# Optimization experiments

Hardware: AMD Instinct MI355X
Metric: run time of the kernel (lower is better)

## Reference

```python
import jax, jax.numpy as jnp
import numpy as np

B, L, D = 4, 4096, 256
INIT_ALPHA = -2.0
INV_TEMP = 1.0 / 0.1


def setup_inputs() -> dict:
    key = jax.random.key(0)
    k1, k2, k3, k4 = jax.random.split(key, 4)
    latents = jax.random.normal(k1, (B, L, D), dtype=jnp.float32)
    current_coords = jax.random.normal(k2, (B, L, 2), dtype=jnp.float32)
    # Linear(D, D, bias=False) weights (torch stores [out, in]; y = x @ W.T)
    lim = 1.0 / np.sqrt(D)
    Wq = jax.random.uniform(k3, (D, D), minval=-lim, maxval=lim, dtype=jnp.float32)
    Wk = jax.random.uniform(k4, (D, D), minval=-lim, maxval=lim, dtype=jnp.float32)
    alpha_raw = jnp.asarray(INIT_ALPHA, dtype=jnp.float32)
    return {"latents": latents, "current_coords": current_coords,
            "Wq": Wq, "Wk": Wk, "alpha_raw": alpha_raw, "layer_idx": 3}


def _l2norm(x, eps=1e-12):
    # F.normalize(dim=-1): x / max(||x||, eps)
    n = jnp.sqrt(jnp.sum(x * x, axis=-1, keepdims=True))
    return x / jnp.maximum(n, eps)


def reference(latents, current_coords, Wq, Wk, alpha_raw, layer_idx):
    # pred_idx selection (share_weights=True): 0 if layer_idx==0 else 1;
    # layer_idx=3 -> params given are for pred_idx=1.
    q = _l2norm(jnp.einsum('bld,ed->ble', latents, Wq))  # [B,L,D]
    k = _l2norm(jnp.einsum('bld,ed->ble', latents, Wk))  # [B,L,D]
    scores = jnp.einsum('bld,bmd->blm', q, k) * INV_TEMP  # [B,L,L]
    scores = jnp.clip(scores, -50.0, 50.0)
    W = jax.nn.softmax(scores, axis=-1)                   # [B,L,L]
    alpha = jax.nn.sigmoid(alpha_raw)
    # M = alpha*W + (1-alpha)*I; M @ coords == alpha*(W@coords) + (1-alpha)*coords
    new_coords = alpha * jnp.einsum('blm,bmc->blc', W, current_coords) \
                 + (1.0 - alpha) * current_coords
    displacement = new_coords - current_coords
    return (new_coords, displacement)
```

## Files before the change

### kernel.cpp

```cpp
#include <hip/hip_runtime.h>
#include <hip/hip_bf16.h>

#define BB 4
#define LL 4096
#define DD 256
#define MM (BB * LL)
#define NSPLIT 8
#define BM 256
#define NQB (LL / BM)
#define KPS (LL / NSPLIT)
#define KT 64
#define NKT (KPS / KT)

typedef short short8 __attribute__((ext_vector_type(8)));
typedef float floatx4 __attribute__((ext_vector_type(4)));

#define SCALE_LOG2E 14.426950408889634f


__device__ __forceinline__ unsigned short f2bf(float f) {
    __hip_bfloat16 h = __float2bfloat16(f);
    union { __hip_bfloat16 h; unsigned short s; } c; c.h = h; return c.s;
}

__device__ __forceinline__ float fast_exp2(float x) {
#if __has_builtin(__builtin_amdgcn_exp2f)
    return __builtin_amdgcn_exp2f(x);
#else
    return exp2f(x);
#endif
}

__device__ __forceinline__ void stage16(const char* g, char* l, int lane) {
#if __has_builtin(__builtin_amdgcn_global_load_lds)
    __builtin_amdgcn_global_load_lds(
        (const __attribute__((address_space(1))) void*)(g + lane * 16),
        (__attribute__((address_space(3))) void*)l, 16, 0, 0);
#else
    *(short8*)(l + lane * 16) = *(const short8*)(g + lane * 16);
#endif
}

__global__ __launch_bounds__(256) void cvt_fm_kernel(
    const float* __restrict__ srcq, const float* __restrict__ srck,
    unsigned short* __restrict__ dstq, unsigned short* __restrict__ dstk)
{
    const int which = blockIdx.x >> 5;
    const float* src = which ? srck : srcq;
    unsigned short* dst = which ? dstk : dstq;
    const int t = (blockIdx.x & 31) * 256 + threadIdx.x;
    const int r = t >> 5, c = t & 31;
    const float4 v0 = ((const float4*)src)[t * 2];
    const float4 v1 = ((const float4*)src)[t * 2 + 1];
    short8 o;
    o[0] = (short)f2bf(v0.x); o[1] = (short)f2bf(v0.y);
    o[2] = (short)f2bf(v0.z); o[3] = (short)f2bf(v0.w);
    o[4] = (short)f2bf(v1.x); o[5] = (short)f2bf(v1.y);
    o[6] = (short)f2bf(v1.z); o[7] = (short)f2bf(v1.w);
    const int chunk = (r >> 4) * 512 + c * 16 + (r & 15);
    *(short8*)(dst + (size_t)chunk * 8) = o;
}

__global__ __launch_bounds__(256) void proj_norm_kernel(
    const float* __restrict__ latents,
    const __hip_bfloat16* __restrict__ Wq,
    const __hip_bfloat16* __restrict__ Wk,
    __hip_bfloat16* __restrict__ qn,
    __hip_bfloat16* __restrict__ kn)
{
    __shared__ char lds[65536];

    const int tid  = threadIdx.x;
    const int wave = tid >> 6;
    const int lane = tid & 63;
    const int n15  = lane & 15;
    const int quad = lane >> 4;

    const int pass  = (blockIdx.x >> 3) & 1;
    const int pidx  = (blockIdx.x & 7) | ((blockIdx.x >> 4) << 3);
    const int rbase = pidx * 64;
    const int m0    = rbase + wave * 16;
    const int r160  = rbase >> 4;

    short8 afrag[8];
    const float* Abase = latents + (size_t)(m0 + n15) * DD + quad * 8;
#pragma unroll
    for (int kk = 0; kk < 8; ++kk) {
        const float4 v0 = *(const float4*)(Abase + kk * 32);
        const float4 v1 = *(const float4*)(Abase + kk * 32 + 4);
        short8 f;
        f[0] = (short)f2bf(v0.x); f[1] = (short)f2bf(v0.y);
        f[2] = (short)f2bf(v0.z); f[3] = (short)f2bf(v0.w);
        f[4] = (short)f2bf(v1.x); f[5] = (short)f2bf(v1.y);
        f[6] = (short)f2bf(v1.z); f[7] = (short)f2bf(v1.w);
        afrag[kk] = f;
    }

    const char* W = (const char*)(pass ? Wk : Wq);

    floatx4 acc[16];
#pragma unroll
    for (int ct = 0; ct < 16; ++ct) acc[ct] = (floatx4){0.f, 0.f, 0.f, 0.f};

    {
        const char* src = W + wave * 8192;
        char* dst = lds + wave * 8192;
#pragma unroll
        for (int j = 0; j < 8; ++j) stage16(src + j * 1024, dst + j * 1024, lane);
    }

    for (int round = 0; round < 4; ++round) {
        __syncthreads();
        if (round + 1 < 4) {
            const char* src = W + (size_t)(round + 1) * 32768 + wave * 8192;
            char* dst = lds + ((round + 1) & 1) * 32768 + wave * 8192;
#pragma unroll
            for (int j = 0; j < 8; ++j) stage16(src + j * 1024, dst + j * 1024, lane);
        }
        const char* buf = lds + (round & 1) * 32768;
#pragma unroll
        for (int jt = 0; jt < 4; ++jt) {
            const int ct = round * 4 + jt;
            const char* lbase = buf + jt * 8192 + lane * 16;
            floatx4 a = acc[ct];
            __builtin_amdgcn_s_setprio(1);
#pragma unroll
            for (int kk = 0; kk < 8; ++kk) {
                short8 bfr = *(const short8*)(lbase + kk * 1024);
                a = __builtin_amdgcn_mfma_f32_16x16x32_bf16(afrag[kk], bfr, a, 0, 0, 0);
            }
            __builtin_amdgcn_s_setprio(0);
            acc[ct] = a;
        }
    }

    float ss[4] = {0.f, 0.f, 0.f, 0.f};
#pragma unroll
    for (int ct = 0; ct < 16; ++ct)
#pragma unroll
        for (int r = 0; r < 4; ++r) ss[r] += acc[ct][r] * acc[ct][r];
#pragma unroll
    for (int r = 0; r < 4; ++r) {
        ss[r] += __shfl_xor(ss[r], 1, 64);
        ss[r] += __shfl_xor(ss[r], 2, 64);
        ss[r] += __shfl_xor(ss[r], 4, 64);
        ss[r] += __shfl_xor(ss[r], 8, 64);
    }
    float sc[4];
#pragma unroll
    for (int r = 0; r < 4; ++r) {
        sc[r] = 1.f / fmaxf(sqrtf(ss[r]), 1e-12f);
        if (pass == 0) sc[r] *= SCALE_LOG2E;
    }

    __hip_bfloat16* dstp = pass ? kn : qn;
    unsigned short* tb = (unsigned short*)lds;
#pragma unroll
    for (int h = 0; h < 2; ++h) {
        __syncthreads();
#pragma unroll
        for (int cth = 0; cth < 8; ++cth) {
            const int ct = h * 8 + cth;
            const int col = cth * 16 + n15;
#pragma unroll
            for (int r = 0; r < 4; ++r) {
                const int rl = wave * 16 + quad * 4 + r;
                tb[rl * 136 + col] = f2bf(acc[ct][r] * sc[r]);
            }
        }
        __syncthreads();
#pragma unroll
        for (int j = 0; j < 4; ++j) {
            const int g = tid + j * 256;
            const int n15r = g & 15, q2 = (g >> 4) & 3, kkh = (g >> 6) & 3, r16l = (g >> 8) & 3;
            const int rl = r16l * 16 + n15r;
            short8 v = *(const short8*)(tb + rl * 136 + kkh * 32 + q2 * 8);
            const size_t chunk = (((size_t)(r160 + r16l) * 8 + (h * 4 + kkh)) * 4 + q2) * 16 + n15r;
            *(short8*)((char*)dstp + chunk * 16) = v;
        }
    }
}

__global__ __launch_bounds__(512) void attn_kernel(
    const __hip_bfloat16* __restrict__ qn,
    const __hip_bfloat16* __restrict__ kn,
    const float* __restrict__ coords,
    float* __restrict__ partials)
{
    __shared__ char lds[2 * 32768];

    const int tid  = threadIdx.x;
    const int wave = tid >> 6;
    const int lane = tid & 63;
    const int n15  = lane & 15;
    const int quad = lane >> 4;

    int bs = (blockIdx.x & 7) * 64 + (blockIdx.x >> 3);
    const int qb    = bs % NQB;    bs /= NQB;
    const int split = bs % NSPLIT; bs /= NSPLIT;
    const int b     = bs;

    const int mw = b * LL + qb * BM + wave * 32;

    const int key_base = b * LL + split * KPS;
    const char* ksrc = (const char*)kn + (size_t)key_base * 512;

    {
        const char* src = ksrc + wave * 4096;
        char* dst = lds + wave * 4096;
#pragma unroll
        for (int j = 0; j < 4; ++j) stage16(src + j * 1024, dst + j * 1024, lane);
    }

    short8 aq[2][8];
    const int t16 = mw >> 4;
#pragma unroll
    for (int rt = 0; rt < 2; ++rt)
#pragma unroll
        for (int kk = 0; kk < 8; ++kk) {
            const size_t chunk = (((size_t)(t16 + rt) * 8 + kk) * 4 + quad) * 16 + n15;
            aq[rt][kk] = *(const short8*)((const char*)qn + chunk * 16);
        }

    float s0[2][4], s1[2][4], s2[2][4];
#pragma unroll
    for (int rt = 0; rt < 2; ++rt)
#pragma unroll
        for (int r = 0; r < 4; ++r) { s0[rt][r] = 0.f; s1[rt][r] = 0.f; s2[rt][r] = 0.f; }

    for (int kt = 0; kt < NKT; ++kt) {
        __syncthreads();
        if (kt + 1 < NKT) {
            const char* src = ksrc + (size_t)(kt + 1) * KT * 512 + wave * 4096;
            char* dst = lds + ((kt + 1) & 1) * 32768 + wave * 4096;
#pragma unroll
            for (int j = 0; j < 4; ++j) stage16(src + j * 1024, dst + j * 1024, lane);
        }
        const char* buf = lds + (kt & 1) * 32768;

#pragma unroll
        for (int ct = 0; ct < 4; ++ct) {
            const int kidx = key_base + kt * KT + ct * 16 + n15;
            const float2 cc = *(const float2*)(coords + (size_t)kidx * 2);

            floatx4 acc[2][2];
#pragma unroll
            for (int rt = 0; rt < 2; ++rt)
#pragma unroll
                for (int hh = 0; hh < 2; ++hh) acc[rt][hh] = (floatx4){0.f, 0.f, 0.f, 0.f};
            const char* lbase = buf + ct * 8192 + lane * 16;
#pragma unroll
            for (int kk = 0; kk < 8; ++kk) {
                const short8 bfr = *(const short8*)(lbase + kk * 1024);
                acc[0][kk >> 2] = __builtin_amdgcn_mfma_f32_16x16x32_bf16(aq[0][kk], bfr, acc[0][kk >> 2], 0, 0, 0);
                acc[1][kk >> 2] = __builtin_amdgcn_mfma_f32_16x16x32_bf16(aq[1][kk], bfr, acc[1][kk >> 2], 0, 0, 0);
            }
#pragma unroll
            for (int r = 0; r < 4; ++r) {
                const float e0 = fast_exp2(acc[0][0][r] + acc[0][1][r]);
                const float e1 = fast_exp2(acc[1][0][r] + acc[1][1][r]);
                s0[0][r] += e0;
                s1[0][r] = fmaf(cc.x, e0, s1[0][r]);
                s2[0][r] = fmaf(cc.y, e0, s2[0][r]);
                s0[1][r] += e1;
                s1[1][r] = fmaf(cc.x, e1, s1[1][r]);
                s2[1][r] = fmaf(cc.y, e1, s2[1][r]);
            }
        }
    }

#pragma unroll
    for (int rt = 0; rt < 2; ++rt)
#pragma unroll
        for (int r = 0; r < 4; ++r)
#pragma unroll
            for (int mask = 1; mask <= 8; mask <<= 1) {
                s0[rt][r] += __shfl_xor(s0[rt][r], mask, 64);
                s1[rt][r] += __shfl_xor(s1[rt][r], mask, 64);
                s2[rt][r] += __shfl_xor(s2[rt][r], mask, 64);
            }

    if (n15 == 0) {
#pragma unroll
        for (int rt = 0; rt < 2; ++rt)
#pragma unroll
            for (int r = 0; r < 4; ++r) {
                const int m = mw + rt * 16 + quad * 4 + r;
                float* p = partials + ((size_t)split * MM + m) * 4;
                p[0] = s0[rt][r];
                p[1] = s1[rt][r];
                p[2] = s2[rt][r];
            }
    }
}

__global__ __launch_bounds__(256) void finish_kernel(
    const float* __restrict__ partials,
    const float* __restrict__ coords,
    const float* __restrict__ alpha_raw,
    float* __restrict__ out)
{
    const int m = blockIdx.x * 256 + threadIdx.x;

    const float alpha = 1.f / (1.f + __expf(-alpha_raw[0]));

    float s0 = 0.f, s1 = 0.f, s2 = 0.f;
#pragma unroll
    for (int s = 0; s < NSPLIT; ++s) {
        const float4 v = *(const float4*)(partials + ((size_t)s * MM + m) * 4);
        s0 += v.x; s1 += v.y; s2 += v.z;
    }

    const float cx = coords[m * 2];
    const float cy = coords[m * 2 + 1];
    const float inv = 1.f / s0;
    const float nx = alpha * (s1 * inv) + (1.f - alpha) * cx;
    const float ny = alpha * (s2 * inv) + (1.f - alpha) * cy;

    out[m * 2]     = nx;
    out[m * 2 + 1] = ny;
    out[2 * MM + m * 2]     = nx - cx;
    out[2 * MM + m * 2 + 1] = ny - cy;
}

extern "C" void kernel_launch(void* const* d_in, const int* in_sizes, int n_in,
                              void* d_out, int out_size, void* d_ws, size_t ws_size,
                              hipStream_t stream) {
    const float* latents   = (const float*)d_in[0];
    const float* coords    = (const float*)d_in[1];
    const float* Wq        = (const float*)d_in[2];
    const float* Wk        = (const float*)d_in[3];
    const float* alpha_raw = (const float*)d_in[4];

    char* ws = (char*)d_ws;
    __hip_bfloat16* qn   = (__hip_bfloat16*)ws;
    __hip_bfloat16* kn   = (__hip_bfloat16*)(ws + (size_t)8 * 1024 * 1024);
    __hip_bfloat16* wq_b = (__hip_bfloat16*)(ws + (size_t)16 * 1024 * 1024);
    __hip_bfloat16* wk_b = (__hip_bfloat16*)(ws + (size_t)16 * 1024 * 1024 + 131072);
    float* partials      = (float*)(ws + (size_t)16 * 1024 * 1024 + 262144);

    float* out = (float*)d_out;

    cvt_fm_kernel<<<64, 256, 0, stream>>>(Wq, Wk, (unsigned short*)wq_b, (unsigned short*)wk_b);
    proj_norm_kernel<<<512, 256, 0, stream>>>(latents, wq_b, wk_b, qn, kn);
    attn_kernel<<<BB * NQB * NSPLIT, 512, 0, stream>>>(qn, kn, coords, partials);
    finish_kernel<<<MM / 256, 256, 0, stream>>>(partials, coords, alpha_raw, out);
}
```

Before: 129.9 us.

## Stage coords in LDS, batch MFMAs over two key tiles with setprio

Each block's coordinate slice for its key split is copied into LDS once at kernel start, so the inner loop no longer issues a global float2 load per 16-key tile. The MFMA chain now runs over two key tiles before the exp/accumulate phase. Each tile uses a single accumulator per row tile instead of two split halves that were added afterwards. s_setprio brackets the MFMA section so waves in that section get issue priority, aiming to overlap matrix work with other waves' exp math. The cost is a longer single dependent MFMA chain per accumulator and slightly more LDS.

```diff
diff --git a/kernel.cpp b/kernel.cpp
--- a/kernel.cpp
+++ b/kernel.cpp
@@ -187,7 +187,8 @@
     const float* __restrict__ coords,
     float* __restrict__ partials)
 {
-    __shared__ char lds[2 * 32768];
+    __shared__ char lds[2 * 32768 + 4096];
+    char* clds = lds + 2 * 32768;
 
     const int tid  = threadIdx.x;
     const int wave = tid >> 6;
@@ -205,6 +206,10 @@
     const int key_base = b * LL + split * KPS;
     const char* ksrc = (const char*)kn + (size_t)key_base * 512;
 
+    if (wave < 4)
+        stage16((const char*)coords + (size_t)key_base * 8 + wave * 1024,
+                clds + wave * 1024, lane);
+
     {
         const char* src = ksrc + wave * 4096;
         char* dst = lds + wave * 4096;
@@ -239,32 +244,41 @@
         const char* buf = lds + (kt & 1) * 32768;
 
 #pragma unroll
-        for (int ct = 0; ct < 4; ++ct) {
-            const int kidx = key_base + kt * KT + ct * 16 + n15;
-            const float2 cc = *(const float2*)(coords + (size_t)kidx * 2);
-
+        for (int ch = 0; ch < 2; ++ch) {
             floatx4 acc[2][2];
 #pragma unroll
-            for (int rt = 0; rt < 2; ++rt)
-#pragma unroll
-                for (int hh = 0; hh < 2; ++hh) acc[rt][hh] = (floatx4){0.f, 0.f, 0.f, 0.f};
-            const char* lbase = buf + ct * 8192 + lane * 16;
-#pragma unroll
-            for (int kk = 0; kk < 8; ++kk) {
-                const short8 bfr = *(const short8*)(lbase + kk * 1024);
-                acc[0][kk >> 2] = __builtin_amdgcn_mfma_f32_16x16x32_bf16(aq[0][kk], bfr, acc[0][kk >> 2], 0, 0, 0);
-                acc[1][kk >> 2] = __builtin_amdgcn_mfma_f32_16x16x32_bf16(aq[1][kk], bfr, acc[1][kk >> 2], 0, 0, 0);
-            }
-#pragma unroll
-            for (int r = 0; r < 4; ++r) {
-                const float e0 = fast_exp2(acc[0][0][r] + acc[0][1][r]);
-                const float e1 = fast_exp2(acc[1][0][r] + acc[1][1][r]);
-                s0[0][r] += e0;
-                s1[0][r] = fmaf(cc.x, e0, s1[0][r]);
-                s2[0][r] = fmaf(cc.y, e0, s2[0][r]);
-                s0[1][r] += e1;
-                s1[1][r] = fmaf(cc.x, e1, s1[1][r]);
-                s2[1][r] = fmaf(cc.y, e1, s2[1][r]);
+            for (int ctl = 0; ctl < 2; ++ctl)
+#pragma unroll
+                for (int rt = 0; rt < 2; ++rt) acc[ctl][rt] = (floatx4){0.f, 0.f, 0.f, 0.f};
+
+            __builtin_amdgcn_s_setprio(1);
+#pragma unroll
+            for (int ctl = 0; ctl < 2; ++ctl) {
+                const char* lbase = buf + (ch * 2 + ctl) * 8192 + lane * 16;
+#pragma unroll
+                for (int kk = 0; kk < 8; ++kk) {
+                    const short8 bfr = *(const short8*)(lbase + kk * 1024);
+                    acc[ctl][0] = __builtin_amdgcn_mfma_f32_16x16x32_bf16(aq[0][kk], bfr, acc[ctl][0], 0, 0, 0);
+                    acc[ctl][1] = __builtin_amdgcn_mfma_f32_16x16x32_bf16(aq[1][kk], bfr, acc[ctl][1], 0, 0, 0);
+                }
+            }
+            __builtin_amdgcn_s_setprio(0);
+
+#pragma unroll
+            for (int ctl = 0; ctl < 2; ++ctl) {
+                const int ct = ch * 2 + ctl;
+                const float2 cc = *(const float2*)(clds + (kt * KT + ct * 16 + n15) * 8);
+#pragma unroll
+                for (int r = 0; r < 4; ++r) {
+                    const float e0 = fast_exp2(acc[ctl][0][r]);
+                    const float e1 = fast_exp2(acc[ctl][1][r]);
+                    s0[0][r] += e0;
+                    s1[0][r] = fmaf(cc.x, e0, s1[0][r]);
+                    s2[0][r] = fmaf(cc.y, e0, s2[0][r]);
+                    s0[1][r] += e1;
+                    s1[1][r] = fmaf(cc.x, e1, s1[1][r]);
+                    s2[1][r] = fmaf(cc.y, e1, s2[1][r]);
+                }
             }
         }
     }
```

Result: faster. 124.9 us (-3.8%).
